# Optimization experiments

Measured on AMD Instinct MI355X. Metric: run time of the kernel, lower is better.

## Reference

```python
import jax, jax.numpy as jnp
import numpy as np

B, NW, NS, SL = 32, 500, 50, 40
EMB, HID, VOCAB, E = 300, 150, 50000, 563200
N = B * (NW + NS)
MAXPOS = 512


def _sinusoid(n_pos, d):
    pos = np.arange(n_pos)[:, None].astype(np.float64)
    i = np.arange(d)[None, :]
    ang = pos / np.power(10000.0, 2 * (i // 2) / d)
    tab = np.zeros((n_pos, d))
    tab[:, 0::2] = np.sin(ang[:, 0::2])
    tab[:, 1::2] = np.cos(ang[:, 1::2])
    tab[0] = 0.0  # padding_idx=0
    return jnp.asarray(tab, dtype=jnp.float32)

_POS_TAB = _sinusoid(MAXPOS + 1, EMB)


def setup_inputs():
    keys = iter(jax.random.split(jax.random.key(0), 48))
    def nrm(shape, s=0.05):
        return jax.random.normal(next(keys), shape, dtype=jnp.float32) * s
    inp = {}
    inp["x"] = jax.random.randint(next(keys), (B, NW), 0, VOCAB, dtype=jnp.int32)
    inp["sent_x"] = jax.random.randint(next(keys), (B, NS, SL), 0, VOCAB, dtype=jnp.int32)
    inp["edge_index"] = jax.random.randint(next(keys), (2, E), 0, N, dtype=jnp.int32)
    inp["embed_table"] = nrm((VOCAB, EMB)).at[0].set(0.0)  # padding_idx=0
    for h in range(2, 8):
        inp["conv_w%d" % h] = nrm((50, 1, h, EMB))
        inp["conv_b%d" % h] = nrm((50,))
    inp["cnn_proj_w"] = nrm((HID, EMB)); inp["cnn_proj_b"] = nrm((HID,))
    inp["lstm_w_ih_l0"] = nrm((2, 4 * HID, HID)); inp["lstm_w_hh_l0"] = nrm((2, 4 * HID, HID))
    inp["lstm_b_ih_l0"] = nrm((2, 4 * HID)); inp["lstm_b_hh_l0"] = nrm((2, 4 * HID))
    inp["lstm_w_ih_l1"] = nrm((2, 4 * HID, 2 * HID)); inp["lstm_w_hh_l1"] = nrm((2, 4 * HID, HID))
    inp["lstm_b_ih_l1"] = nrm((2, 4 * HID)); inp["lstm_b_hh_l1"] = nrm((2, 4 * HID))
    inp["lstm_proj_w"] = nrm((HID, 2 * HID)); inp["lstm_proj_b"] = nrm((HID,))
    inp["gc0_w"] = nrm((HID, EMB)); inp["gc0_b"] = nrm((HID,))
    inp["gc1_w"] = nrm((HID, HID)); inp["gc1_b"] = nrm((HID,))
    inp["gc2_w"] = nrm((HID, HID)); inp["gc2_b"] = nrm((HID,))
    return inp


def _forward(x, sent_x, edge_index, embed_table, conv_ws, conv_bs,
             cnn_proj_w, cnn_proj_b, w_ih0, w_hh0, b_ih0, b_hh0,
             w_ih1, w_hh1, b_ih1, b_hh1, lstm_proj_w, lstm_proj_b,
             gc0_w, gc0_b, gc1_w, gc1_b, gc2_w, gc2_b):
    Bsz, S, L = sent_x.shape
    Nn = Bsz * S
    emb_words = embed_table[x]                                   # [B, NW, EMB]
    tok = embed_table[sent_x].reshape(Nn, L, EMB)                # [Nn, L, EMB]
    sentlen = (sent_x != 0).sum(-1).reshape(Nn)                  # token count per sentence
    a = jnp.arange(L)
    input_pos = jnp.where(a[None, :] < sentlen[:, None], a[None, :] + 1, 0)
    enc = tok + _POS_TAB[input_pos]
    # CNN ngram features: conv heights 2..7, full-width kernels == windowed matmuls
    feats = []
    for w, b in zip(conv_ws, conv_bs):
        h = w.shape[2]
        acc = b + sum(jnp.einsum('nld,od->nlo', enc[:, k:L - h + 1 + k, :], w[:, 0, k, :]) for k in range(h))
        feats.append(jnp.max(jax.nn.relu(acc), axis=1))          # [Nn, 50]
    ngram = jnp.concatenate(feats, axis=1)                        # [Nn, 300]
    snode_pos = jnp.tile(jnp.arange(S), Bsz)
    cnn_feat = ((ngram + _POS_TAB[snode_pos]) @ cnn_proj_w.T + cnn_proj_b).reshape(Bsz, S, HID)
    glen = (sent_x[:, :, 0] != 0).sum(-1)                         # valid sentence count per graph

    def lstm_dir(xs, w_ih, w_hh, bias):
        def step(carry, xt):
            hh, cc = carry
            g = xt @ w_ih.T + hh @ w_hh.T + bias
            i, f, gg, o = jnp.split(g, 4, axis=-1)
            cc = jax.nn.sigmoid(f) * cc + jax.nn.sigmoid(i) * jnp.tanh(gg)
            hh = jax.nn.sigmoid(o) * jnp.tanh(cc)
            return (hh, cc), hh
        z = jnp.zeros((xs.shape[0], HID), xs.dtype)
        _, hs = jax.lax.scan(step, (z, z), jnp.swapaxes(xs, 0, 1))
        return jnp.swapaxes(hs, 0, 1)

    def rev_within(xs):
        # reverse only the first glen[b] steps (packed-sequence semantics)
        T = xs.shape[1]; t = jnp.arange(T)
        idx = jnp.where(t[None, :] < glen[:, None], glen[:, None] - 1 - t[None, :], t[None, :])
        return jnp.take_along_axis(xs, idx[:, :, None], axis=1)

    def bidir(xs, w_ih, w_hh, b_i, b_h):
        f = lstm_dir(xs, w_ih[0], w_hh[0], b_i[0] + b_h[0])
        r = rev_within(lstm_dir(rev_within(xs), w_ih[1], w_hh[1], b_i[1] + b_h[1]))
        return jnp.concatenate([f, r], axis=-1)

    h1 = bidir(cnn_feat, w_ih0, w_hh0, b_ih0, b_hh0)
    h2 = bidir(h1, w_ih1, w_hh1, b_ih1, b_hh1)
    mask = (jnp.arange(S)[None, :] < glen[:, None]).astype(h2.dtype)[:, :, None]
    lstm_feat = (h2 * mask) @ lstm_proj_w.T + lstm_proj_b
    sent_out = jnp.concatenate([cnn_feat, lstm_feat], axis=-1)    # [B, S, 300]
    nodes = jnp.concatenate([emb_words, sent_out], axis=1)        # [B, NW+S, 300]
    nodes = (nodes @ gc0_w.T + gc0_b).reshape(-1, HID)            # [N, 150]
    Nt = nodes.shape[0]
    loop = jnp.arange(Nt, dtype=edge_index.dtype)
    src = jnp.concatenate([edge_index[0], loop])                  # add self-loops
    dst = jnp.concatenate([edge_index[1], loop])
    deg = jax.ops.segment_sum(jnp.ones(src.shape[0], nodes.dtype), dst, num_segments=Nt)
    dis = jnp.where(deg > 0, jax.lax.rsqrt(deg), 0.0)
    norm = (dis[src] * dis[dst])[:, None]

    def gcn(xin, w, bias):
        xw = xin @ w.T
        return jax.ops.segment_sum(xw[src] * norm, dst, num_segments=Nt) + bias

    h = jax.nn.elu(gcn(nodes, gc1_w, gc1_b))
    # F.dropout with training=False -> identity
    return gcn(h, gc2_w, gc2_b), emb_words


def reference(x, sent_x, edge_index, embed_table, conv_w2, conv_b2, conv_w3, conv_b3,
              conv_w4, conv_b4, conv_w5, conv_b5, conv_w6, conv_b6, conv_w7, conv_b7,
              cnn_proj_w, cnn_proj_b, lstm_w_ih_l0, lstm_w_hh_l0, lstm_b_ih_l0, lstm_b_hh_l0,
              lstm_w_ih_l1, lstm_w_hh_l1, lstm_b_ih_l1, lstm_b_hh_l1, lstm_proj_w, lstm_proj_b,
              gc0_w, gc0_b, gc1_w, gc1_b, gc2_w, gc2_b):
    conv_ws = [conv_w2, conv_w3, conv_w4, conv_w5, conv_w6, conv_w7]
    conv_bs = [conv_b2, conv_b3, conv_b4, conv_b5, conv_b6, conv_b7]
    return _forward(x, sent_x, edge_index, embed_table, conv_ws, conv_bs,
                    cnn_proj_w, cnn_proj_b, lstm_w_ih_l0, lstm_w_hh_l0, lstm_b_ih_l0, lstm_b_hh_l0,
                    lstm_w_ih_l1, lstm_w_hh_l1, lstm_b_ih_l1, lstm_b_hh_l1, lstm_proj_w, lstm_proj_b,
                    gc0_w, gc0_b, gc1_w, gc1_b, gc2_w, gc2_b)
```

## Files before the change

### kernel.cpp

```cpp
#include <hip/hip_runtime.h>
#include <stdint.h>
#include <math.h>

#define EDGES 563200
#define NNODES 17600
#define OUT0SZ 2640000
#define MROWS 64000
#define MPAD  64016
#define KSTRIDE 2112

typedef _Float16 h2 __attribute__((ext_vector_type(2)));
typedef _Float16 h4 __attribute__((ext_vector_type(4)));
typedef _Float16 v8h __attribute__((ext_vector_type(8)));
typedef float v4f __attribute__((ext_vector_type(4)));

__device__ __forceinline__ float sigm(float x){ return 1.f / (1.f + expf(-x)); }

__device__ __forceinline__ float fdot2_(h2 a, h2 b, float c){
#if __has_builtin(__builtin_amdgcn_fdot2)
  return __builtin_amdgcn_fdot2(a, b, c, false);
#else
  return c + (float)a.x * (float)b.x + (float)a.y * (float)b.y;
#endif
}

__device__ __forceinline__ void stage16(const char* g, char* lds_base, int lane){
#if __has_builtin(__builtin_amdgcn_global_load_lds)
  __builtin_amdgcn_global_load_lds(
      (const __attribute__((address_space(1))) void*)g,
      (__attribute__((address_space(3))) void*)lds_base, 16, 0, 0);
#else
  uint4 v = *(const uint4*)g;
  *(uint4*)(lds_base + lane * 16) = v;
#endif
}

__global__ __launch_bounds__(1024)
void gcnk_prep2(const int* __restrict__ sx, int* __restrict__ sentlen,
                int* __restrict__ glen_g, int* __restrict__ rowmap){
  __shared__ int sg[32];
  int tid = threadIdx.x;
  for (int i = tid; i < 1600; i += 1024){
    int c = 0;
    for (int j = 0; j < 40; j++) c += (sx[i * 40 + j] != 0);
    sentlen[i] = c;
  }
  if (tid < 32){
    int c = 0;
    for (int s = 0; s < 50; s++) c += (sx[tid * 2000 + s * 40] != 0);
    glen_g[tid] = c; sg[tid] = c;
  }
  __syncthreads();
  for (int i = tid; i < 1600; i += 1024){
    int b = i / 50, t = i - b * 50, g = sg[b];
    rowmap[i] = b * 50 + ((t < g) ? (g - 1 - t) : t);
  }
}

__global__ __launch_bounds__(256)
void gcnk_mergedprep(float* __restrict__ pos,
                     const float* w2, const float* w3, const float* w4,
                     const float* w5, const float* w6, const float* w7,
                     const float* c2, const float* c3, const float* c4,
                     const float* c5, const float* c6, const float* c7,
                     _Float16* __restrict__ Bp, float* __restrict__ bias_p,
                     const float* __restrict__ whh0, _Float16* __restrict__ wpad0,
                     const float* __restrict__ whh1, _Float16* __restrict__ wpad1,
                     unsigned int* __restrict__ ngram_u, unsigned int* __restrict__ ecnt_u,
                     const int* __restrict__ x, const float* __restrict__ tab,
                     float4* __restrict__ out1){
  int blk = blockIdx.x, tid = threadIdx.x;
  if (blk < 602){
    int idx = blk * 256 + tid;
    if (idx >= 513 * 300) return;
    int p = idx / 300, i = idx - p * 300;
    float v = 0.f;
    if (p != 0){
      double expo = (double)(2 * (i / 2)) / 300.0;
      double ang = (double)p / pow(10000.0, expo);
      v = (float)((i & 1) ? cos(ang) : sin(ang));
    }
    pos[idx] = v;
  } else if (blk < 3242){
    int idx = (blk - 602) * 256 + tid;
    if (idx < 2 * 160 * KSTRIDE){
      int n = idx / KSTRIDE, kk = idx - n * KSTRIDE;
      int g = n / 160, c = n - g * 160;
      _Float16 v = (_Float16)0.f;
      if (c < 150){
        int H = 3 * g + 2 + c / 50, o = c % 50;
        if (kk < 300 * H){
          const float* w;
          switch (H){ case 2: w = w2; break; case 3: w = w3; break;
                      case 4: w = w4; break; case 5: w = w5; break;
                      case 6: w = w6; break; default: w = w7; break; }
          v = (_Float16)w[o * 300 * H + kk];
        }
      }
      Bp[idx] = v;
    }
    if (idx < 320){
      int g = idx / 160, c = idx - g * 160;
      float bv = 0.f;
      if (c < 150){
        int H = 3 * g + 2 + c / 50, o = c % 50;
        const float* cbp;
        switch (H){ case 2: cbp = c2; break; case 3: cbp = c3; break;
                    case 4: cbp = c4; break; case 5: cbp = c5; break;
                    case 6: cbp = c6; break; default: cbp = c7; break; }
        bv = cbp[o];
      }
      bias_p[idx] = bv;
    }
  } else if (blk < 3955){
    int idx = (blk - 3242) * 256 + tid;
    if (idx >= 1200 * 152) return;
    int row = idx / 152, col = idx - row * 152;
    wpad0[idx] = (col < 150) ? (_Float16)whh0[row * 150 + col] : (_Float16)0.f;
  } else if (blk < 4668){
    int idx = (blk - 3955) * 256 + tid;
    if (idx >= 1200 * 152) return;
    int row = idx / 152, col = idx - row * 152;
    wpad1[idx] = (col < 150) ? (_Float16)whh1[row * 150 + col] : (_Float16)0.f;
  } else if (blk < 6543){
    int idx = (blk - 4668) * 256 + tid;
    if (idx < 1600 * 300) ngram_u[idx] = 0u;
  } else if (blk < 6612){
    int idx = (blk - 6543) * 256 + tid;
    if (idx < NNODES) ecnt_u[idx] = 0u;
  } else {
    int idx = (blk - 6612) * 256 + tid;
    if (idx >= 16000 * 75) return;
    int row = idx / 75, q = idx - row * 75;
    const float4* t = (const float4*)tab;
    out1[idx] = t[x[row] * 75 + q];
  }
}

__global__ void gcnk_ench(const int* __restrict__ sx, const float* __restrict__ tab,
                          const float* __restrict__ pos, const int* __restrict__ sentlen,
                          _Float16* __restrict__ ench){
  int idx = blockIdx.x * 256 + threadIdx.x;
  if (idx >= MPAD * 75) return;
  int row = idx / 75, q = idx - row * 75;
  int d = q * 4;
  h4 o; o[0] = (_Float16)0.f; o[1] = (_Float16)0.f; o[2] = (_Float16)0.f; o[3] = (_Float16)0.f;
  if (row < MROWS){
    int n = row / 40, l = row - n * 40;
    int tok = sx[n * 40 + l];
    int p = (l < sentlen[n]) ? (l + 1) : 0;
    float4 a = *(const float4*)(tab + (size_t)tok * 300 + d);
    float4 b = *(const float4*)(pos + (size_t)p * 300 + d);
    o[0] = (_Float16)(a.x + b.x); o[1] = (_Float16)(a.y + b.y);
    o[2] = (_Float16)(a.z + b.z); o[3] = (_Float16)(a.w + b.w);
  }
  *(h4*)(ench + (size_t)row * 300 + d) = o;
}

__global__ __launch_bounds__(256)
void gcnk_convmfma(const _Float16* __restrict__ A, const _Float16* __restrict__ Bp,
                   const float* __restrict__ bias_p, unsigned int* __restrict__ ngram_u){
  __shared__ __align__(1024) char smem[36864];
  _Float16* Asm = (_Float16*)smem;
  _Float16* Bsm = (_Float16*)(smem + 16384);
  float* Cs = (float*)smem;
  const int tid = threadIdx.x;
  const int bid = blockIdx.x;
  const int work = (bid & 7) * 125 + (bid >> 3);
  const int m0 = (work >> 1) * 128;
  const int grp = (work & 1) ^ ((work >> 5) & 1);
  const char* Abase = (const char*)A;
  const char* Bbase = (const char*)(Bp + (size_t)grp * 160 * KSTRIDE);
  const int kmax = grp ? 2112 : 1216;
  const int w = tid >> 6, lane = tid & 63;
  const int wm = (w >> 1) * 64, wn = (w & 1) * 80;
  const int fm = lane & 15, fq = lane >> 4;
  const int lrow = lane >> 3;
  const int loff = (((lane & 7) ^ lrow) << 4);

  v4f acc[4][5] = {};

  for (int kc = 0; kc < kmax; kc += 64){
    #pragma unroll
    for (int ii = 0; ii < 4; ii++){
      int i = w * 4 + ii;
      const char* g = Abase + (size_t)(m0 + i * 8 + lrow) * 600 + kc * 2 + loff;
      stage16(g, (char*)Asm + i * 1024, lane);
    }
    #pragma unroll
    for (int jj = 0; jj < 5; jj++){
      int j = w * 5 + jj;
      const char* g = Bbase + (size_t)(j * 8 + lrow) * (KSTRIDE * 2) + kc * 2 + loff;
      stage16(g, (char*)Bsm + j * 1024, lane);
    }
    __syncthreads();
    #pragma unroll
    for (int ks = 0; ks < 2; ks++){
      const int axor = (ks * 64 + fq * 16) ^ ((fm & 7) << 4);
      v8h af[4], bf[5];
      #pragma unroll
      for (int mt = 0; mt < 4; mt++)
        af[mt] = *(const v8h*)((const char*)Asm + (wm + mt * 16 + fm) * 128 + axor);
      #pragma unroll
      for (int nt = 0; nt < 5; nt++)
        bf[nt] = *(const v8h*)((const char*)Bsm + (wn + nt * 16 + fm) * 128 + axor);
      #pragma unroll
      for (int mt = 0; mt < 4; mt++)
        #pragma unroll
        for (int nt = 0; nt < 5; nt++)
          acc[mt][nt] = __builtin_amdgcn_mfma_f32_16x16x32_f16(af[mt], bf[nt], acc[mt][nt], 0, 0, 0);
    }
    __syncthreads();
  }

  for (int p = 0; p < 5; p++){
    __syncthreads();
    #pragma unroll
    for (int nt = 0; nt < 5; nt++){
      int cstart = wn + nt * 16;
      if ((cstart >> 5) == p){
        int co = cstart - p * 32 + fm;
        #pragma unroll
        for (int mt = 0; mt < 4; mt++)
          #pragma unroll
          for (int r = 0; r < 4; r++)
            Cs[(wm + mt * 16 + fq * 4 + r) * 33 + co] = acc[mt][nt][r];
      }
    }
    __syncthreads();
    if (tid < 128){
      int cl = tid & 31, si = tid >> 5;
      int col = p * 32 + cl;
      if (col < 150){
        int H = 3 * grp + 2 + col / 50, lh = 41 - H;
        int sent = m0 / 40 + si;
        if (sent < 1600){
          int rlo = sent * 40; if (rlo < m0) rlo = m0;
          int rhi = sent * 40 + lh; if (rhi > m0 + 128) rhi = m0 + 128;
          if (rlo < rhi){
            float bv = bias_p[grp * 160 + col];
            float vmax = 0.f;
            for (int r = rlo; r < rhi; r++){
              float v = Cs[(r - m0) * 33 + cl] + bv;
              vmax = fmaxf(vmax, v);
            }
            atomicMax(ngram_u + sent * 300 + grp * 150 + col, __float_as_uint(vmax));
          }
        }
      }
    }
  }
}

template<int BM, int BN, int WMT, int WNT, int OUTH>
__global__ __launch_bounds__(256)
void gcnk_mgemm(const float* __restrict__ A, const float* __restrict__ Wt,
                const float* __restrict__ b1, const float* __restrict__ b2,
                void* __restrict__ Cv, int M, int N, int K){
  __shared__ __align__(16) _Float16 As[BM * 40];
  __shared__ __align__(16) _Float16 Bs[BN * 40];
  const int tid = threadIdx.x;
  const int m0 = blockIdx.x * BM, n0 = blockIdx.y * BN;
  const int w = tid >> 6, lane = tid & 63;
  const int wm = (w >> 1) * (WMT * 16), wn = (w & 1) * (WNT * 16);
  const int fm = lane & 15, fq = lane >> 4;
  v4f acc[WMT][WNT] = {};
  const int nch = (K + 31) >> 5;
  for (int ch = 0; ch < nch; ch++){
    int kc = ch * 32;
    #pragma unroll
    for (int j = 0; j < BM / 64; j++){
      int u = tid + 256 * j;
      int row = u >> 2, cb = (u & 3) * 8;
      int gm = m0 + row, gk = kc + cb;
      v8h vv;
      if (gm < M && gk + 8 <= K){
        const float2* p = (const float2*)(A + (size_t)gm * K + gk);
        float2 q0 = p[0], q1 = p[1], q2 = p[2], q3 = p[3];
        vv[0] = (_Float16)q0.x; vv[1] = (_Float16)q0.y;
        vv[2] = (_Float16)q1.x; vv[3] = (_Float16)q1.y;
        vv[4] = (_Float16)q2.x; vv[5] = (_Float16)q2.y;
        vv[6] = (_Float16)q3.x; vv[7] = (_Float16)q3.y;
      } else {
        #pragma unroll
        for (int e = 0; e < 8; e++)
          vv[e] = (gm < M && gk + e < K) ? (_Float16)A[(size_t)gm * K + gk + e] : (_Float16)0.f;
      }
      *(v8h*)(As + row * 40 + cb) = vv;
    }
    {
      int row = tid >> 2, cb = (tid & 3) * 8;
      int gn = n0 + row, gk = kc + cb;
      v8h vv;
      if (gn < N && gk + 8 <= K){
        const float2* p = (const float2*)(Wt + (size_t)gn * K + gk);
        float2 q0 = p[0], q1 = p[1], q2 = p[2], q3 = p[3];
        vv[0] = (_Float16)q0.x; vv[1] = (_Float16)q0.y;
        vv[2] = (_Float16)q1.x; vv[3] = (_Float16)q1.y;
        vv[4] = (_Float16)q2.x; vv[5] = (_Float16)q2.y;
        vv[6] = (_Float16)q3.x; vv[7] = (_Float16)q3.y;
      } else {
        #pragma unroll
        for (int e = 0; e < 8; e++)
          vv[e] = (gn < N && gk + e < K) ? (_Float16)Wt[(size_t)gn * K + gk + e] : (_Float16)0.f;
      }
      *(v8h*)(Bs + row * 40 + cb) = vv;
    }
    __syncthreads();
    v8h af[WMT], bf[WNT];
    #pragma unroll
    for (int mt = 0; mt < WMT; mt++)
      af[mt] = *(const v8h*)(As + (wm + mt * 16 + fm) * 40 + fq * 8);
    #pragma unroll
    for (int nt = 0; nt < WNT; nt++)
      bf[nt] = *(const v8h*)(Bs + (wn + nt * 16 + fm) * 40 + fq * 8);
    #pragma unroll
    for (int mt = 0; mt < WMT; mt++)
      #pragma unroll
      for (int nt = 0; nt < WNT; nt++)
        acc[mt][nt] = __builtin_amdgcn_mfma_f32_16x16x32_f16(af[mt], bf[nt], acc[mt][nt], 0, 0, 0);
    __syncthreads();
  }
  #pragma unroll
  for (int nt = 0; nt < WNT; nt++){
    int gn = n0 + wn + nt * 16 + fm;
    if (gn >= N) continue;
    float badd = (b1 ? b1[gn] : 0.f) + (b2 ? b2[gn] : 0.f);
    #pragma unroll
    for (int mt = 0; mt < WMT; mt++)
      #pragma unroll
      for (int r = 0; r < 4; r++){
        int gm = m0 + wm + mt * 16 + fq * 4 + r;
        if (gm < M){
          float val = acc[mt][nt][r] + badd;
          if (OUTH) ((_Float16*)Cv)[(size_t)gm * 160 + gn] = (_Float16)val;
          else      ((float*)Cv)[(size_t)gm * N + gn] = val;
        }
      }
  }
}

__global__ __launch_bounds__(256)
void gcnk_mgemmH(const _Float16* __restrict__ Ah, const float* __restrict__ Wt,
                 const float* __restrict__ b1, float* __restrict__ C, int M, int N){
  const int K = 300;
  __shared__ __align__(16) _Float16 As[128 * 40];
  __shared__ __align__(16) _Float16 Bs[64 * 40];
  const int tid = threadIdx.x;
  const int m0 = blockIdx.x * 128, n0 = blockIdx.y * 64;
  const int w = tid >> 6, lane = tid & 63;
  const int wm = (w >> 1) * 64, wn = (w & 1) * 32;
  const int fm = lane & 15, fq = lane >> 4;
  v4f acc[4][2] = {};
  for (int ch = 0; ch < 10; ch++){
    int kc = ch * 32;
    #pragma unroll
    for (int j = 0; j < 2; j++){
      int u = tid + 256 * j;
      int row = u >> 2, cb = (u & 3) * 8;
      int gm = m0 + row, gk = kc + cb;
      v8h vv;
      if (gm < M && gk + 8 <= K){
        const char* p = (const char*)(Ah + (size_t)gm * 300 + gk);
        union { uint2 u2[2]; v8h v; } t;
        t.u2[0] = *(const uint2*)p; t.u2[1] = *(const uint2*)(p + 8);
        vv = t.v;
      } else {
        #pragma unroll
        for (int e = 0; e < 8; e++)
          vv[e] = (gm < M && gk + e < K) ? Ah[(size_t)gm * 300 + gk + e] : (_Float16)0.f;
      }
      *(v8h*)(As + row * 40 + cb) = vv;
    }
    {
      int row = tid >> 2, cb = (tid & 3) * 8;
      int gn = n0 + row, gk = kc + cb;
      v8h vv;
      if (gn < N && gk + 8 <= K){
        const float2* p = (const float2*)(Wt + (size_t)gn * K + gk);
        float2 q0 = p[0], q1 = p[1], q2 = p[2], q3 = p[3];
        vv[0] = (_Float16)q0.x; vv[1] = (_Float16)q0.y;
        vv[2] = (_Float16)q1.x; vv[3] = (_Float16)q1.y;
        vv[4] = (_Float16)q2.x; vv[5] = (_Float16)q2.y;
        vv[6] = (_Float16)q3.x; vv[7] = (_Float16)q3.y;
      } else {
        #pragma unroll
        for (int e = 0; e < 8; e++)
          vv[e] = (gn < N && gk + e < K) ? (_Float16)Wt[(size_t)gn * K + gk + e] : (_Float16)0.f;
      }
      *(v8h*)(Bs + row * 40 + cb) = vv;
    }
    __syncthreads();
    v8h af[4], bf[2];
    #pragma unroll
    for (int mt = 0; mt < 4; mt++)
      af[mt] = *(const v8h*)(As + (wm + mt * 16 + fm) * 40 + fq * 8);
    #pragma unroll
    for (int nt = 0; nt < 2; nt++)
      bf[nt] = *(const v8h*)(Bs + (wn + nt * 16 + fm) * 40 + fq * 8);
    #pragma unroll
    for (int mt = 0; mt < 4; mt++)
      #pragma unroll
      for (int nt = 0; nt < 2; nt++)
        acc[mt][nt] = __builtin_amdgcn_mfma_f32_16x16x32_f16(af[mt], bf[nt], acc[mt][nt], 0, 0, 0);
    __syncthreads();
  }
  #pragma unroll
  for (int nt = 0; nt < 2; nt++){
    int gn = n0 + wn + nt * 16 + fm;
    if (gn >= N) continue;
    float badd = b1[gn];
    #pragma unroll
    for (int mt = 0; mt < 4; mt++)
      #pragma unroll
      for (int r = 0; r < 4; r++){
        int gm = m0 + wm + mt * 16 + fq * 4 + r;
        if (gm < M) C[(size_t)gm * N + gn] = acc[mt][nt][r] + badd;
      }
  }
}

__global__ __launch_bounds__(256)
void gcnk_mgemmF(const float* __restrict__ A1, const int* __restrict__ mapA,
                 const float* __restrict__ A2, const int* __restrict__ mapB,
                 const int* __restrict__ glen, int usemask,
                 const float* __restrict__ apos,
                 const float* __restrict__ Wt, const float* __restrict__ b1,
                 const float* __restrict__ b2, float* __restrict__ C,
                 int M, int N, int K){
  const int BM = 64, WMT = 2, WNT = 2;
  __shared__ __align__(16) _Float16 As[BM * 40];
  __shared__ __align__(16) _Float16 Bs[64 * 40];
  const int tid = threadIdx.x;
  const int m0 = blockIdx.x * BM, n0 = blockIdx.y * 64;
  const int w = tid >> 6, lane = tid & 63;
  const int wm = (w >> 1) * (WMT * 16), wn = (w & 1) * (WNT * 16);
  const int fm = lane & 15, fq = lane >> 4;
  v4f acc[WMT][WNT] = {};
  const int nch = (K + 31) >> 5;
  for (int ch = 0; ch < nch; ch++){
    int kc = ch * 32;
    {
      int row = tid >> 2, cb = (tid & 3) * 8;
      int gm = m0 + row, gk = kc + cb;
      v8h vv;
      bool ok = (gm < M);
      if (ok && usemask){
        int b = gm / 50;
        if (gm - b * 50 >= glen[b]) ok = false;
      }
      if (!ok){
        #pragma unroll
        for (int e = 0; e < 8; e++) vv[e] = (_Float16)0.f;
      } else if (!A2){
        int r = mapA ? mapA[gm] : gm;
        const float* base = A1 + (size_t)r * K;
        if (gk + 8 <= K){
          const float2* p = (const float2*)(base + gk);
          float2 q0 = p[0], q1 = p[1], q2 = p[2], q3 = p[3];
          if (apos){
            const float2* a2 = (const float2*)(apos + (size_t)(gm % 50) * K + gk);
            float2 r0 = a2[0], r1 = a2[1], r2 = a2[2], r3 = a2[3];
            q0.x += r0.x; q0.y += r0.y; q1.x += r1.x; q1.y += r1.y;
            q2.x += r2.x; q2.y += r2.y; q3.x += r3.x; q3.y += r3.y;
          }
          vv[0] = (_Float16)q0.x; vv[1] = (_Float16)q0.y;
          vv[2] = (_Float16)q1.x; vv[3] = (_Float16)q1.y;
          vv[4] = (_Float16)q2.x; vv[5] = (_Float16)q2.y;
          vv[6] = (_Float16)q3.x; vv[7] = (_Float16)q3.y;
        } else {
          #pragma unroll
          for (int e = 0; e < 8; e++){
            int c = gk + e;
            float vf = (c < K) ? base[c] : 0.f;
            if (apos && c < K) vf += apos[(size_t)(gm % 50) * K + c];
            vv[e] = (_Float16)vf;
          }
        }
      } else {
        int rA = mapA ? mapA[gm] : gm;
        int rB = mapB ? mapB[gm] : gm;
        const float* pa = A1 + (size_t)rA * 150;
        const float* pb = A2 + (size_t)rB * 150;
        if (gk + 8 <= 150){
          const float2* p = (const float2*)(pa + gk);
          float2 q0 = p[0], q1 = p[1], q2 = p[2], q3 = p[3];
          vv[0] = (_Float16)q0.x; vv[1] = (_Float16)q0.y;
          vv[2] = (_Float16)q1.x; vv[3] = (_Float16)q1.y;
          vv[4] = (_Float16)q2.x; vv[5] = (_Float16)q2.y;
          vv[6] = (_Float16)q3.x; vv[7] = (_Float16)q3.y;
        } else if (gk >= 152 && gk + 8 <= K){
          const float2* p = (const float2*)(pb + gk - 150);
          float2 q0 = p[0], q1 = p[1], q2 = p[2], q3 = p[3];
          vv[0] = (_Float16)q0.x; vv[1] = (_Float16)q0.y;
          vv[2] = (_Float16)q1.x; vv[3] = (_Float16)q1.y;
          vv[4] = (_Float16)q2.x; vv[5] = (_Float16)q2.y;
          vv[6] = (_Float16)q3.x; vv[7] = (_Float16)q3.y;
        } else {
          #pragma unroll
          for (int e = 0; e < 8; e++){
            int c = gk + e;
            vv[e] = (c < 150) ? (_Float16)pa[c]
                  : ((c < K) ? (_Float16)pb[c - 150] : (_Float16)0.f);
          }
        }
      }
      *(v8h*)(As + row * 40 + cb) = vv;
    }
    {
      int row = tid >> 2, cb = (tid & 3) * 8;
      int gn = n0 + row, gk = kc + cb;
      v8h vv;
      if (gn < N && gk + 8 <= K){
        const float2* p = (const float2*)(Wt + (size_t)gn * K + gk);
        float2 q0 = p[0], q1 = p[1], q2 = p[2], q3 = p[3];
        vv[0] = (_Float16)q0.x; vv[1] = (_Float16)q0.y;
        vv[2] = (_Float16)q1.x; vv[3] = (_Float16)q1.y;
        vv[4] = (_Float16)q2.x; vv[5] = (_Float16)q2.y;
        vv[6] = (_Float16)q3.x; vv[7] = (_Float16)q3.y;
      } else {
        #pragma unroll
        for (int e = 0; e < 8; e++)
          vv[e] = (gn < N && gk + e < K) ? (_Float16)Wt[(size_t)gn * K + gk + e] : (_Float16)0.f;
      }
      *(v8h*)(Bs + row * 40 + cb) = vv;
    }
    __syncthreads();
    v8h af[WMT], bf[WNT];
    #pragma unroll
    for (int mt = 0; mt < WMT; mt++)
      af[mt] = *(const v8h*)(As + (wm + mt * 16 + fm) * 40 + fq * 8);
    #pragma unroll
    for (int nt = 0; nt < WNT; nt++)
      bf[nt] = *(const v8h*)(Bs + (wn + nt * 16 + fm) * 40 + fq * 8);
    #pragma unroll
    for (int mt = 0; mt < WMT; mt++)
      #pragma unroll
      for (int nt = 0; nt < WNT; nt++)
        acc[mt][nt] = __builtin_amdgcn_mfma_f32_16x16x32_f16(af[mt], bf[nt], acc[mt][nt], 0, 0, 0);
    __syncthreads();
  }
  #pragma unroll
  for (int nt = 0; nt < WNT; nt++){
    int gn = n0 + wn + nt * 16 + fm;
    if (gn >= N) continue;
    float badd = (b1 ? b1[gn] : 0.f) + (b2 ? b2[gn] : 0.f);
    #pragma unroll
    for (int mt = 0; mt < WMT; mt++)
      #pragma unroll
      for (int r = 0; r < 4; r++){
        int gm = m0 + wm + mt * 16 + fq * 4 + r;
        if (gm < M) C[(size_t)gm * N + gn] = acc[mt][nt][r] + badd;
      }
  }
}

__global__ void gcnk_nodes_in_h(const int* __restrict__ x, const float* __restrict__ tab,
                                const float* __restrict__ cnnf, const float* __restrict__ lstmf,
                                h2* __restrict__ out){
  int idx = blockIdx.x * 256 + threadIdx.x;
  if (idx >= NNODES * 150) return;
  int nrow = idx / 150, q = idx - nrow * 150;
  int d = q * 2;
  int b = nrow / 550, j = nrow - b * 550;
  float2 v;
  if (j < 500) v = *(const float2*)(tab + (size_t)x[b * 500 + j] * 300 + d);
  else {
    int r = b * 50 + (j - 500);
    if (d < 150) v = *(const float2*)(cnnf + (size_t)r * 150 + d);
    else         v = *(const float2*)(lstmf + (size_t)r * 150 + d - 150);
  }
  h2 o; o[0] = (_Float16)v.x; o[1] = (_Float16)v.y;
  out[idx] = o;
}

__global__ __launch_bounds__(640)
void gcnk_lstm(const float* __restrict__ xf, const float* __restrict__ xr,
               const _Float16* __restrict__ wpad, float* __restrict__ fo,
               float* __restrict__ ro){
  int b = blockIdx.x >> 1, dir = blockIdx.x & 1;
  const float* xih = dir ? xr : xf;
  float* out = dir ? ro : fo;
  __shared__ __align__(16) _Float16 hh[160];
  __shared__ float gates[600];
  const int tid = threadIdx.x;

  h2 w[76];
  if (tid < 600){
    const h2* wrow = (const h2*)(wpad + ((size_t)dir * 600 + tid) * 152);
    #pragma unroll
    for (int j = 0; j < 76; j++) w[j] = wrow[j];
  }
  for (int u = tid; u < 160; u += 640) hh[u] = (_Float16)0.f;
  float creg = 0.f;
  __syncthreads();

  for (int t = 0; t < 50; t++){
    if (tid < 600){
      float acc = xih[(b * 50 + t) * 600 + tid];
      float a0 = 0.f, a1 = 0.f, a2 = 0.f, a3 = 0.f;
      #pragma unroll
      for (int j = 0; j < 19; j++){
        union { float4 f; h2 h[4]; } u;
        u.f = *(const float4*)(hh + j * 8);
        a0 = fdot2_(w[4 * j + 0], u.h[0], a0);
        a1 = fdot2_(w[4 * j + 1], u.h[1], a1);
        a2 = fdot2_(w[4 * j + 2], u.h[2], a2);
        a3 = fdot2_(w[4 * j + 3], u.h[3], a3);
      }
      gates[tid] = acc + ((a0 + a1) + (a2 + a3));
    }
    __syncthreads();
    if (tid < 150){
      float ig = sigm(gates[tid]);
      float fg = sigm(gates[150 + tid]);
      float gg = tanhf(gates[300 + tid]);
      float og = sigm(gates[450 + tid]);
      creg = fg * creg + ig * gg;
      float hn = og * tanhf(creg);
      hh[tid] = (_Float16)hn;
      out[(b * 50 + t) * 150 + tid] = hn;
    }
    __syncthreads();
  }
}

__global__ void gcnk_hist(const int* __restrict__ ei, int* __restrict__ ecnt){
  int e = blockIdx.x * 256 + threadIdx.x;
  if (e < EDGES) atomicAdd(&ecnt[ei[EDGES + e]], 1);
}

__global__ __launch_bounds__(1024)
void gcnk_scan(const int* __restrict__ ecnt, int* __restrict__ eoff,
               int* __restrict__ ecur, float* __restrict__ dis){
  __shared__ int wsum[16];
  int tid = threadIdx.x;
  int base = tid * 18;
  int pre[18];
  int s = 0;
  #pragma unroll
  for (int i = 0; i < 18; i++){
    int idx = base + i;
    int c = (idx < NNODES) ? ecnt[idx] : 0;
    if (idx < NNODES) dis[idx] = rsqrtf((float)(c + 1));
    pre[i] = s; s += c;
  }
  int lane = tid & 63, wid = tid >> 6;
  int run = s;
  #pragma unroll
  for (int off = 1; off < 64; off <<= 1){
    int y = __shfl_up(run, off, 64);
    if (lane >= off) run += y;
  }
  if (lane == 63) wsum[wid] = run;
  __syncthreads();
  if (tid == 0){
    int a = 0;
    #pragma unroll
    for (int i = 0; i < 16; i++){ int t2 = wsum[i]; wsum[i] = a; a += t2; }
  }
  __syncthreads();
  int excl = wsum[wid] + run - s;
  #pragma unroll
  for (int i = 0; i < 18; i++){
    int idx = base + i;
    if (idx < NNODES){
      int e = excl + pre[i];
      eoff[idx] = e; ecur[idx] = e;
    }
  }
}

__global__ void gcnk_scatter(const int* __restrict__ ei, int* __restrict__ ecur,
                             int* __restrict__ esrc){
  int e = blockIdx.x * 256 + threadIdx.x;
  if (e < EDGES){
    int d = ei[EDGES + e];
    int p = atomicAdd(&ecur[d], 1);
    esrc[p] = ei[e];
  }
}

__global__ __launch_bounds__(128)
void gcnk_aggcsr_h(const int* __restrict__ eoff, const int* __restrict__ ecnt,
                   const int* __restrict__ esrc, const float* __restrict__ dis,
                   const _Float16* __restrict__ xw, const float* __restrict__ bias,
                   float* __restrict__ out, int doelu){
  int d = blockIdx.x, t = threadIdx.x;
  float dd = dis[d];
  bool act = t < 75;
  float ax0 = 0.f, ay0 = 0.f, ax1 = 0.f, ay1 = 0.f;
  if (act){
    h2 v = *(const h2*)(xw + (size_t)d * 160 + 2 * t);
    ax0 = (float)v[0] * dd; ay0 = (float)v[1] * dd;
  }
  int beg = eoff[d], end = beg + ecnt[d];
  int j = beg;
  for (; j + 1 < end; j += 2){
    int s0 = esrc[j], s1 = esrc[j + 1];
    float d0 = dis[s0], d1 = dis[s1];
    if (act){
      h2 v0 = *(const h2*)(xw + (size_t)s0 * 160 + 2 * t);
      h2 v1 = *(const h2*)(xw + (size_t)s1 * 160 + 2 * t);
      ax0 += (float)v0[0] * d0; ay0 += (float)v0[1] * d0;
      ax1 += (float)v1[0] * d1; ay1 += (float)v1[1] * d1;
    }
  }
  if (j < end){
    int s = esrc[j];
    float ds_ = dis[s];
    if (act){
      h2 v = *(const h2*)(xw + (size_t)s * 160 + 2 * t);
      ax0 += (float)v[0] * ds_; ay0 += (float)v[1] * ds_;
    }
  }
  if (act){
    float o0 = (ax0 + ax1) * dd + bias[2 * t];
    float o1 = (ay0 + ay1) * dd + bias[2 * t + 1];
    if (doelu){
      o0 = (o0 > 0.f) ? o0 : expm1f(o0);
      o1 = (o1 > 0.f) ? o1 : expm1f(o1);
    }
    *(float2*)(out + (size_t)d * 150 + 2 * t) = make_float2(o0, o1);
  }
}

extern "C" void kernel_launch(void* const* d_in, const int* in_sizes, int n_in,
                              void* d_out, int out_size, void* d_ws, size_t ws_size,
                              hipStream_t stream){
  (void)in_sizes; (void)n_in; (void)out_size; (void)ws_size;

  char* wsb = (char*)d_ws;
  size_t off = 0;
  auto alloc = [&](size_t bytes) -> void* {
    void* p = wsb + off;
    off = (off + bytes + 255) & ~(size_t)255;
    return p;
  };
  float* pos_tab  = (float*)alloc(513 * 300 * 4);
  int*   sentlen  = (int*)alloc(1600 * 4);
  int*   glen     = (int*)alloc(32 * 4);
  int*   rowmap   = (int*)alloc(1600 * 4);
  float* ngram    = (float*)alloc(1600 * 300 * 4);
  float* cnn_feat = (float*)alloc(1600 * 150 * 4);
  float* xih_f    = (float*)alloc(1600 * 600 * 4);
  float* xih_r    = (float*)alloc(1600 * 600 * 4);
  float* f0       = (float*)alloc(1600 * 150 * 4);
  float* r0       = (float*)alloc(1600 * 150 * 4);
  float* f1       = (float*)alloc(1600 * 150 * 4);
  float* r1       = (float*)alloc(1600 * 150 * 4);
  float* lstm_ft  = (float*)alloc(1600 * 150 * 4);
  h2*    nodes_ih = (h2*)alloc((size_t)NNODES * 150 * 4);
  float* nodes    = (float*)alloc((size_t)NNODES * 150 * 4);
  float* dis      = (float*)alloc(NNODES * 4);
  _Float16* xwh   = (_Float16*)alloc((size_t)NNODES * 160 * 2);
  _Float16* ench  = (_Float16*)alloc((size_t)MPAD * 300 * 2);
  _Float16* Bp    = (_Float16*)alloc((size_t)2 * 160 * KSTRIDE * 2);
  float* bias_p   = (float*)alloc(320 * 4);
  _Float16* wpad0 = (_Float16*)alloc(1200 * 152 * 2);
  _Float16* wpad1 = (_Float16*)alloc(1200 * 152 * 2);
  int*   ecnt     = (int*)alloc(NNODES * 4);
  int*   eoff     = (int*)alloc(NNODES * 4);
  int*   ecur     = (int*)alloc(NNODES * 4);
  int*   esrc     = (int*)alloc(EDGES * 4);

  const int*   x   = (const int*)d_in[0];
  const int*   sx  = (const int*)d_in[1];
  const int*   ei  = (const int*)d_in[2];
  const float* tab = (const float*)d_in[3];
  const float *cw[6], *cb[6];
  for (int h = 0; h < 6; h++){ cw[h] = (const float*)d_in[4 + 2 * h]; cb[h] = (const float*)d_in[5 + 2 * h]; }
  const float* cnnw = (const float*)d_in[16]; const float* cnnb = (const float*)d_in[17];
  const float* wih0 = (const float*)d_in[18]; const float* whh0 = (const float*)d_in[19];
  const float* bih0 = (const float*)d_in[20]; const float* bhh0 = (const float*)d_in[21];
  const float* wih1 = (const float*)d_in[22]; const float* whh1 = (const float*)d_in[23];
  const float* bih1 = (const float*)d_in[24]; const float* bhh1 = (const float*)d_in[25];
  const float* lpw  = (const float*)d_in[26]; const float* lpb  = (const float*)d_in[27];
  const float* g0w  = (const float*)d_in[28]; const float* g0b  = (const float*)d_in[29];
  const float* g1w  = (const float*)d_in[30]; const float* g1b  = (const float*)d_in[31];
  const float* g2w  = (const float*)d_in[32]; const float* g2b  = (const float*)d_in[33];

  float* out0 = (float*)d_out;
  float4* out1 = (float4*)((float*)d_out + OUT0SZ);

  auto mgemmLH = [&](const float* A, const float* W, void* C, int M, int N, int K){
    dim3 g((M + 127) / 128, (N + 63) / 64);
    gcnk_mgemm<128, 64, 4, 2, 1><<<g, 256, 0, stream>>>(A, W, nullptr, nullptr, C, M, N, K);
  };
  auto mgemmF = [&](const float* A1, const int* mapA, const float* A2, const int* mapB,
                    const int* gl, int um, const float* apos, const float* W,
                    const float* b1, const float* b2, float* C, int N, int K){
    dim3 g(25, (N + 63) / 64);
    gcnk_mgemmF<<<g, 256, 0, stream>>>(A1, mapA, A2, mapB, gl, um, apos, W, b1, b2, C, 1600, N, K);
  };

  gcnk_prep2<<<1, 1024, 0, stream>>>(sx, sentlen, glen, rowmap);
  gcnk_mergedprep<<<11300, 256, 0, stream>>>(
      pos_tab, cw[0], cw[1], cw[2], cw[3], cw[4], cw[5],
      cb[0], cb[1], cb[2], cb[3], cb[4], cb[5], Bp, bias_p,
      whh0, wpad0, whh1, wpad1, (unsigned int*)ngram, (unsigned int*)ecnt,
      x, tab, out1);
  gcnk_ench<<<(MPAD * 75 + 255) / 256, 256, 0, stream>>>(sx, tab, pos_tab, sentlen, ench);

  gcnk_convmfma<<<1000, 256, 0, stream>>>(ench, Bp, bias_p, (unsigned int*)ngram);

  mgemmF(ngram, nullptr, nullptr, nullptr, nullptr, 0, pos_tab,
         cnnw, cnnb, nullptr, cnn_feat, 150, 300);

  mgemmF(cnn_feat, nullptr, nullptr, nullptr, nullptr, 0, nullptr,
         wih0,             bih0,       bhh0,       xih_f, 600, 150);
  mgemmF(cnn_feat, rowmap,  nullptr, nullptr, nullptr, 0, nullptr,
         wih0 + 600 * 150, bih0 + 600, bhh0 + 600, xih_r, 600, 150);
  gcnk_lstm<<<64, 640, 0, stream>>>(xih_f, xih_r, wpad0, f0, r0);

  mgemmF(f0, nullptr, r0, rowmap, nullptr, 0, nullptr,
         wih1,             bih1,       bhh1,       xih_f, 600, 300);
  mgemmF(f0, rowmap, r0, nullptr, nullptr, 0, nullptr,
         wih1 + 600 * 300, bih1 + 600, bhh1 + 600, xih_r, 600, 300);
  gcnk_lstm<<<64, 640, 0, stream>>>(xih_f, xih_r, wpad1, f1, r1);

  mgemmF(f1, nullptr, r1, rowmap, glen, 1, nullptr, lpw, lpb, nullptr, lstm_ft, 150, 300);

  gcnk_nodes_in_h<<<(NNODES * 150 + 255) / 256, 256, 0, stream>>>(x, tab, cnn_feat, lstm_ft, nodes_ih);
  {
    dim3 g(138, 3);
    gcnk_mgemmH<<<g, 256, 0, stream>>>((const _Float16*)nodes_ih, g0w, g0b, nodes, NNODES, 150);
  }

  gcnk_hist<<<2200, 256, 0, stream>>>(ei, ecnt);
  gcnk_scan<<<1, 1024, 0, stream>>>(ecnt, eoff, ecur, dis);
  gcnk_scatter<<<2200, 256, 0, stream>>>(ei, ecur, esrc);

  mgemmLH(nodes, g1w, xwh, NNODES, 150, 150);
  gcnk_aggcsr_h<<<NNODES, 128, 0, stream>>>(eoff, ecnt, esrc, dis, xwh, g1b, nodes, 1);

  mgemmLH(nodes, g2w, xwh, NNODES, 150, 150);
  gcnk_aggcsr_h<<<NNODES, 128, 0, stream>>>(eoff, ecnt, esrc, dis, xwh, g2b, out0, 0);
}
```

Baseline: 793.3 us.

## Batch forward/reverse LSTM input GEMMs into one launch; simplify conv block mapping

Adds a gcnk_mgemmF2 kernel that handles the forward and reverse LSTM input projections for each layer in one launch, choosing the parameter set by blockIdx.z. This replaces two launches per layer and puts more blocks in flight at once. The conv MFMA kernel also drops its swizzled block-to-work mapping for a plain 2D grid (row tile, group). That may change L2 locality and load balance between the two K-length groups.

```diff
diff --git a/kernel.cpp b/kernel.cpp
--- a/kernel.cpp
+++ b/kernel.cpp
@@ -165,10 +165,8 @@
   _Float16* Bsm = (_Float16*)(smem + 16384);
   float* Cs = (float*)smem;
   const int tid = threadIdx.x;
-  const int bid = blockIdx.x;
-  const int work = (bid & 7) * 125 + (bid >> 3);
-  const int m0 = (work >> 1) * 128;
-  const int grp = (work & 1) ^ ((work >> 5) & 1);
+  const int m0 = blockIdx.x * 128;
+  const int grp = blockIdx.y;
   const char* Abase = (const char*)A;
   const char* Bbase = (const char*)(Bp + (size_t)grp * 160 * KSTRIDE);
   const int kmax = grp ? 2112 : 1216;
@@ -555,6 +553,128 @@
   }
 }
 
+struct FArgs {
+  const float* A1; const int* mapA;
+  const float* A2; const int* mapB;
+  const float* Wt; const float* b1; const float* b2;
+  float* C;
+};
+
+__global__ __launch_bounds__(256)
+void gcnk_mgemmF2(FArgs pa, FArgs pb, int M, int N, int K){
+  const int BM = 64, WMT = 2, WNT = 2;
+  __shared__ __align__(16) _Float16 As[BM * 40];
+  __shared__ __align__(16) _Float16 Bs[64 * 40];
+  const FArgs P = blockIdx.z ? pb : pa;
+  const int tid = threadIdx.x;
+  const int m0 = blockIdx.x * BM, n0 = blockIdx.y * 64;
+  const int w = tid >> 6, lane = tid & 63;
+  const int wm = (w >> 1) * (WMT * 16), wn = (w & 1) * (WNT * 16);
+  const int fm = lane & 15, fq = lane >> 4;
+  v4f acc[WMT][WNT] = {};
+  const int nch = (K + 31) >> 5;
+  for (int ch = 0; ch < nch; ch++){
+    int kc = ch * 32;
+    {
+      int row = tid >> 2, cb = (tid & 3) * 8;
+      int gm = m0 + row, gk = kc + cb;
+      v8h vv;
+      if (gm >= M){
+        #pragma unroll
+        for (int e = 0; e < 8; e++) vv[e] = (_Float16)0.f;
+      } else if (!P.A2){
+        int r = P.mapA ? P.mapA[gm] : gm;
+        const float* base = P.A1 + (size_t)r * K;
+        if (gk + 8 <= K){
+          const float2* p = (const float2*)(base + gk);
+          float2 q0 = p[0], q1 = p[1], q2 = p[2], q3 = p[3];
+          vv[0] = (_Float16)q0.x; vv[1] = (_Float16)q0.y;
+          vv[2] = (_Float16)q1.x; vv[3] = (_Float16)q1.y;
+          vv[4] = (_Float16)q2.x; vv[5] = (_Float16)q2.y;
+          vv[6] = (_Float16)q3.x; vv[7] = (_Float16)q3.y;
+        } else {
+          #pragma unroll
+          for (int e = 0; e < 8; e++)
+            vv[e] = (gk + e < K) ? (_Float16)base[gk + e] : (_Float16)0.f;
+        }
+      } else {
+        int rA = P.mapA ? P.mapA[gm] : gm;
+        int rB = P.mapB ? P.mapB[gm] : gm;
+        const float* paa = P.A1 + (size_t)rA * 150;
+        const float* pbb = P.A2 + (size_t)rB * 150;
+        if (gk + 8 <= 150){
+          const float2* p = (const float2*)(paa + gk);
+          float2 q0 = p[0], q1 = p[1], q2 = p[2], q3 = p[3];
+          vv[0] = (_Float16)q0.x; vv[1] = (_Float16)q0.y;
+          vv[2] = (_Float16)q1.x; vv[3] = (_Float16)q1.y;
+          vv[4] = (_Float16)q2.x; vv[5] = (_Float16)q2.y;
+          vv[6] = (_Float16)q3.x; vv[7] = (_Float16)q3.y;
+        } else if (gk >= 152 && gk + 8 <= K){
+          const float2* p = (const float2*)(pbb + gk - 150);
+          float2 q0 = p[0], q1 = p[1], q2 = p[2], q3 = p[3];
+          vv[0] = (_Float16)q0.x; vv[1] = (_Float16)q0.y;
+          vv[2] = (_Float16)q1.x; vv[3] = (_Float16)q1.y;
+          vv[4] = (_Float16)q2.x; vv[5] = (_Float16)q2.y;
+          vv[6] = (_Float16)q3.x; vv[7] = (_Float16)q3.y;
+        } else {
+          #pragma unroll
+          for (int e = 0; e < 8; e++){
+            int c = gk + e;
+            vv[e] = (c < 150) ? (_Float16)paa[c]
+                  : ((c < K) ? (_Float16)pbb[c - 150] : (_Float16)0.f);
+          }
+        }
+      }
+      *(v8h*)(As + row * 40 + cb) = vv;
+    }
+    {
+      int row = tid >> 2, cb = (tid & 3) * 8;
+      int gn = n0 + row, gk = kc + cb;
+      v8h vv;
+      if (gn < N && gk + 8 <= K){
+        const float2* p = (const float2*)(P.Wt + (size_t)gn * K + gk);
+        float2 q0 = p[0], q1 = p[1], q2 = p[2], q3 = p[3];
+        vv[0] = (_Float16)q0.x; vv[1] = (_Float16)q0.y;
+        vv[2] = (_Float16)q1.x; vv[3] = (_Float16)q1.y;
+        vv[4] = (_Float16)q2.x; vv[5] = (_Float16)q2.y;
+        vv[6] = (_Float16)q3.x; vv[7] = (_Float16)q3.y;
+      } else {
+        #pragma unroll
+        for (int e = 0; e < 8; e++)
+          vv[e] = (gn < N && gk + e < K) ? (_Float16)P.Wt[(size_t)gn * K + gk + e] : (_Float16)0.f;
+      }
+      *(v8h*)(Bs + row * 40 + cb) = vv;
+    }
+    __syncthreads();
+    v8h af[WMT], bf[WNT];
+    #pragma unroll
+    for (int mt = 0; mt < WMT; mt++)
+      af[mt] = *(const v8h*)(As + (wm + mt * 16 + fm) * 40 + fq * 8);
+    #pragma unroll
+    for (int nt = 0; nt < WNT; nt++)
+      bf[nt] = *(const v8h*)(Bs + (wn + nt * 16 + fm) * 40 + fq * 8);
+    #pragma unroll
+    for (int mt = 0; mt < WMT; mt++)
+      #pragma unroll
+      for (int nt = 0; nt < WNT; nt++)
+        acc[mt][nt] = __builtin_amdgcn_mfma_f32_16x16x32_f16(af[mt], bf[nt], acc[mt][nt], 0, 0, 0);
+    __syncthreads();
+  }
+  #pragma unroll
+  for (int nt = 0; nt < WNT; nt++){
+    int gn = n0 + wn + nt * 16 + fm;
+    if (gn >= N) continue;
+    float badd = (P.b1 ? P.b1[gn] : 0.f) + (P.b2 ? P.b2[gn] : 0.f);
+    #pragma unroll
+    for (int mt = 0; mt < WMT; mt++)
+      #pragma unroll
+      for (int r = 0; r < 4; r++){
+        int gm = m0 + wm + mt * 16 + fq * 4 + r;
+        if (gm < M) P.C[(size_t)gm * N + gn] = acc[mt][nt][r] + badd;
+      }
+  }
+}
+
 __global__ void gcnk_nodes_in_h(const int* __restrict__ x, const float* __restrict__ tab,
                                 const float* __restrict__ cnnf, const float* __restrict__ lstmf,
                                 h2* __restrict__ out){
@@ -802,21 +922,28 @@
       x, tab, out1);
   gcnk_ench<<<(MPAD * 75 + 255) / 256, 256, 0, stream>>>(sx, tab, pos_tab, sentlen, ench);
 
-  gcnk_convmfma<<<1000, 256, 0, stream>>>(ench, Bp, bias_p, (unsigned int*)ngram);
+  {
+    dim3 g(500, 2);
+    gcnk_convmfma<<<g, 256, 0, stream>>>(ench, Bp, bias_p, (unsigned int*)ngram);
+  }
 
   mgemmF(ngram, nullptr, nullptr, nullptr, nullptr, 0, pos_tab,
          cnnw, cnnb, nullptr, cnn_feat, 150, 300);
 
-  mgemmF(cnn_feat, nullptr, nullptr, nullptr, nullptr, 0, nullptr,
-         wih0,             bih0,       bhh0,       xih_f, 600, 150);
-  mgemmF(cnn_feat, rowmap,  nullptr, nullptr, nullptr, 0, nullptr,
-         wih0 + 600 * 150, bih0 + 600, bhh0 + 600, xih_r, 600, 150);
+  {
+    FArgs pa{cnn_feat, nullptr, nullptr, nullptr, wih0,             bih0,       bhh0,       xih_f};
+    FArgs pb{cnn_feat, rowmap,  nullptr, nullptr, wih0 + 600 * 150, bih0 + 600, bhh0 + 600, xih_r};
+    dim3 g(25, 10, 2);
+    gcnk_mgemmF2<<<g, 256, 0, stream>>>(pa, pb, 1600, 600, 150);
+  }
   gcnk_lstm<<<64, 640, 0, stream>>>(xih_f, xih_r, wpad0, f0, r0);
 
-  mgemmF(f0, nullptr, r0, rowmap, nullptr, 0, nullptr,
-         wih1,             bih1,       bhh1,       xih_f, 600, 300);
-  mgemmF(f0, rowmap, r0, nullptr, nullptr, 0, nullptr,
-         wih1 + 600 * 300, bih1 + 600, bhh1 + 600, xih_r, 600, 300);
+  {
+    FArgs pa{f0, nullptr, r0, rowmap,  wih1,             bih1,       bhh1,       xih_f};
+    FArgs pb{f0, rowmap,  r0, nullptr, wih1 + 600 * 300, bih1 + 600, bhh1 + 600, xih_r};
+    dim3 g(25, 10, 2);
+    gcnk_mgemmF2<<<g, 256, 0, stream>>>(pa, pb, 1600, 600, 300);
+  }
   gcnk_lstm<<<64, 640, 0, stream>>>(xih_f, xih_r, wpad1, f1, r1);
 
   mgemmF(f1, nullptr, r1, rowmap, glen, 1, nullptr, lpw, lpb, nullptr, lstm_ft, 150, 300);
```

Result: faster. 769.2 us (-3.0%).
